# Kernel optimization log

Hardware: AMD Instinct MI355X
Metric: run time of the kernel (lower is better)

Reference implementation:

```python
import jax, jax.numpy as jnp
import numpy as np

HEADS = 4
DIM_HEAD = 32


def setup_inputs() -> dict:
    key = jax.random.key(0)
    k1, k2, k3 = jax.random.split(key, 3)
    b, c, d, h, w = 2, 64, 48, 48, 48
    hidden = HEADS * DIM_HEAD  # 128
    x = jax.random.normal(k1, (b, c, d, h, w), dtype=jnp.float32)
    # 1x1x1 convs are pointwise linear maps over channels
    w_qkv = jax.random.normal(k2, (hidden * 3, c), dtype=jnp.float32) * (1.0 / np.sqrt(c))
    w_out = jax.random.normal(k3, (c, hidden), dtype=jnp.float32) * (1.0 / np.sqrt(hidden))
    b_out = jnp.zeros((c,), dtype=jnp.float32)
    return {"x": x, "w_qkv": w_qkv, "w_out": w_out, "b_out": b_out}


def reference(x, w_qkv, w_out, b_out):
    b, c, d, h, w = x.shape
    n = d * h * w
    xf = x.reshape(b, c, n)                                # [b,c,n]
    qkv = jnp.einsum('oc,bcn->bon', w_qkv, xf)             # [b,3*heads*dh,n]
    qkv = qkv.reshape(b, 3, HEADS, DIM_HEAD, n)            # split order: qkv, heads, c
    q, k, v = qkv[:, 0], qkv[:, 1], qkv[:, 2]              # each [b,heads,dh,n]
    k = jax.nn.softmax(k, axis=-1)
    context = jnp.einsum('bhdn,bhen->bhde', k, v)          # [b,heads,dh,dh]
    out = jnp.einsum('bhde,bhdn->bhen', context, q)        # [b,heads,dh,n]
    out = out.reshape(b, HEADS * DIM_HEAD, n)
    out = jnp.einsum('co,bon->bcn', w_out, out) + b_out[None, :, None]
    return out.reshape(b, c, d, h, w)
```

## Files before the change

kernel.cpp:

```cpp
#include <hip/hip_runtime.h>
#include <stdint.h>


using f32x4 = __attribute__((ext_vector_type(4))) float;
using s16x8 = __attribute__((ext_vector_type(8))) short;

#define NSP 110592
#define NSHADOW 16
#define MFMA(a, b, c) __builtin_amdgcn_mfma_f32_16x16x32_bf16((a), (b), (c), 0, 0, 0)

static __device__ __forceinline__ unsigned short f2bf(float f) {
    return (unsigned short)((__float_as_uint(f) + 0x8000u) >> 16);
}

__global__ __launch_bounds__(256, 4) void k1z(
    const float* __restrict__ x, const float* __restrict__ wqkv,
    float* __restrict__ Sdst, float* __restrict__ Zdst, int mode)
{
    __shared__ unsigned short XT[64][68];
    __shared__ unsigned short EKV[4][2][32][40];
    const int tid = threadIdx.x;
    const int wv = tid >> 6;
    const int l = tid & 63;
    const int l15 = l & 15, l4 = l >> 4;
    const int blk = blockIdx.x;
    const int b = blk / 576;
    const int tbase = (blk % 576) * 6;
    const int h = wv;

    s16x8 afr[2][2][2];
    for (int kv = 0; kv < 2; ++kv)
        for (int mt = 0; mt < 2; ++mt)
            for (int s = 0; s < 2; ++s) {
                int row = 128 + kv * 128 + h * 32 + mt * 16 + l15;
                const float* wp = wqkv + row * 64 + s * 32 + l4 * 8;
                s16x8 a;
#pragma unroll
                for (int j = 0; j < 8; ++j) a[j] = (short)f2bf(wp[j]);
                afr[kv][mt][s] = a;
            }

    f32x4 sacc[2][2] = {};
    float zrow[8] = {};

    unsigned short (*EK)[40] = EKV[wv][0];
    unsigned short (*EV)[40] = EKV[wv][1];
    const float* xb = x + (size_t)b * 64 * NSP;

    const int c0 = tid >> 3;
    const int ng0 = (tid & 7) ^ (c0 & 7);
    const int c1 = (tid + 256) >> 3;
    const int ng1 = ((tid + 256) & 7) ^ (c1 & 7);

    float4 g0, g1;
    {
        const int n0 = tbase * 32;
        g0 = *(const float4*)(xb + (size_t)c0 * NSP + n0 + 4 * ng0);
        g1 = *(const float4*)(xb + (size_t)c1 * NSP + n0 + 4 * ng1);
    }

    for (int it = 0; it < 6; ++it) {
        if (it > 0) __syncthreads();
        {
            ushort4 u0, u1;
            u0.x = f2bf(g0.x); u0.y = f2bf(g0.y); u0.z = f2bf(g0.z); u0.w = f2bf(g0.w);
            u1.x = f2bf(g1.x); u1.y = f2bf(g1.y); u1.z = f2bf(g1.z); u1.w = f2bf(g1.w);
            *(ushort4*)&XT[c0][4 * ng0] = u0;
            *(ushort4*)&XT[c1][4 * ng1] = u1;
        }
        if (it < 5) {
            const int n0 = (tbase + it + 1) * 32;
            g0 = *(const float4*)(xb + (size_t)c0 * NSP + n0 + 4 * ng0);
            g1 = *(const float4*)(xb + (size_t)c1 * NSP + n0 + 4 * ng1);
        }
        __syncthreads();

        f32x4 ck[2][2] = {}, cv[2][2] = {};
#pragma unroll
        for (int s = 0; s < 2; ++s)
#pragma unroll
            for (int nt = 0; nt < 2; ++nt) {
                s16x8 bfr;
#pragma unroll
                for (int j = 0; j < 8; ++j)
                    bfr[j] = (short)XT[s * 32 + l4 * 8 + j][nt * 16 + l15];
#pragma unroll
                for (int mt = 0; mt < 2; ++mt) {
                    ck[mt][nt] = MFMA(afr[0][mt][s], bfr, ck[mt][nt]);
                    cv[mt][nt] = MFMA(afr[1][mt][s], bfr, cv[mt][nt]);
                }
            }
#pragma unroll
        for (int mt = 0; mt < 2; ++mt)
#pragma unroll
            for (int nt = 0; nt < 2; ++nt) {
                int col = nt * 16 + l15;
#pragma unroll
                for (int r = 0; r < 4; ++r) {
                    int row = mt * 16 + l4 * 4 + r;
                    float ek = __expf(ck[mt][nt][r]);
                    zrow[mt * 4 + r] += ek;
                    EK[row][col] = f2bf(ek);
                    EV[row][col] = f2bf(cv[mt][nt][r]);
                }
            }
#pragma unroll
        for (int td = 0; td < 2; ++td) {
            s16x8 a2 = *(const s16x8*)&EK[td * 16 + l15][l4 * 8];
#pragma unroll
            for (int te = 0; te < 2; ++te) {
                s16x8 b2 = *(const s16x8*)&EV[te * 16 + l15][l4 * 8];
                sacc[td][te] = MFMA(a2, b2, sacc[td][te]);
            }
        }
    }

#pragma unroll
    for (int i = 0; i < 8; ++i) {
        float z = zrow[i];
        z += __shfl_xor(z, 1);
        z += __shfl_xor(z, 2);
        z += __shfl_xor(z, 4);
        z += __shfl_xor(z, 8);
        zrow[i] = z;
    }

    if (mode == 0) {
        float* Zb = Zdst + (size_t)blk * 128;
        if (l15 == 0)
#pragma unroll
            for (int mt = 0; mt < 2; ++mt)
#pragma unroll
                for (int r = 0; r < 4; ++r)
                    Zb[h * 32 + mt * 16 + l4 * 4 + r] = zrow[mt * 4 + r];
        float* Sb = Sdst + (size_t)blk * 4096 + h * 1024;
#pragma unroll
        for (int td = 0; td < 2; ++td)
#pragma unroll
            for (int te = 0; te < 2; ++te)
#pragma unroll
                for (int r = 0; r < 4; ++r)
                    Sb[(td * 16 + l4 * 4 + r) * 32 + te * 16 + l15] =
                        sacc[td][te][r];
    } else {
        const int shadow = blk & (NSHADOW - 1);
        float* Zb = Zdst + (size_t)(shadow * 2 + b) * 128;
        if (l15 == 0)
#pragma unroll
            for (int mt = 0; mt < 2; ++mt)
#pragma unroll
                for (int r = 0; r < 4; ++r)
                    atomicAdd(&Zb[h * 32 + mt * 16 + l4 * 4 + r], zrow[mt * 4 + r]);
        float* Sb = Sdst + (size_t)(shadow * 2 + b) * 4096 + h * 1024;
#pragma unroll
        for (int td = 0; td < 2; ++td)
#pragma unroll
            for (int te = 0; te < 2; ++te)
#pragma unroll
                for (int r = 0; r < 4; ++r)
                    atomicAdd(&Sb[(td * 16 + l4 * 4 + r) * 32 + te * 16 + l15],
                              sacc[td][te][r]);
    }
}

__global__ __launch_bounds__(256) void k2pre(
    const float* __restrict__ Sp, const float* __restrict__ Zp,
    float* __restrict__ Ssh, float* __restrict__ Zsh)
{
    const int q = blockIdx.x & 3;
    const int b = (blockIdx.x >> 2) & 1;
    const int s = blockIdx.x >> 3;
    const int t = threadIdx.x;
    const int i = q * 1024 + t * 4;
    float4 acc = {0.f, 0.f, 0.f, 0.f};
#pragma unroll 6
    for (int j = 0; j < 36; ++j) {
        const float4 v =
            *(const float4*)&Sp[(size_t)(b * 576 + s + 16 * j) * 4096 + i];
        acc.x += v.x; acc.y += v.y; acc.z += v.z; acc.w += v.w;
    }
    *(float4*)&Ssh[(size_t)(s * 2 + b) * 4096 + i] = acc;
    if (q == 0 && t < 128) {
        float z = 0.f;
#pragma unroll 6
        for (int j = 0; j < 36; ++j)
            z += Zp[(size_t)(b * 576 + s + 16 * j) * 128 + t];
        Zsh[(size_t)(s * 2 + b) * 128 + t] = z;
    }
}

__global__ __launch_bounds__(1024) void k2s(
    const float* __restrict__ Ssh, const float* __restrict__ Zsh,
    const float* __restrict__ wout, const float* __restrict__ wqkv,
    unsigned short* __restrict__ WE)
{
    __shared__ float ctx[4][32][32];
    __shared__ float P[64][128];
    __shared__ float Zl[128];
    const int b = blockIdx.x;
    const int t = threadIdx.x;
    if (t < 128) {
        float z = 0.f;
#pragma unroll
        for (int s = 0; s < NSHADOW; ++s) z += Zsh[(size_t)(s * 2 + b) * 128 + t];
        Zl[t] = z;
    }
    __syncthreads();
    for (int i = t; i < 4096; i += 1024) {
        float sv = 0.f;
#pragma unroll
        for (int s = 0; s < NSHADOW; ++s) sv += Ssh[(size_t)(s * 2 + b) * 4096 + i];
        int h = i >> 10, d = (i >> 5) & 31;
        ctx[h][d][i & 31] = sv / Zl[h * 32 + d];
    }
    __syncthreads();
    for (int i = t; i < 8192; i += 1024) {
        int c = i >> 7, hd = i & 127, h = hd >> 5, d = hd & 31;
        const float* wo = wout + c * 128 + h * 32;
        float acc = 0.f;
#pragma unroll 8
        for (int e = 0; e < 32; ++e) acc += wo[e] * ctx[h][d][e];
        P[c][hd] = acc;
    }
    __syncthreads();
    for (int i = t; i < 4096; i += 1024) {
        int c = i >> 6, c2 = i & 63;
        float acc = 0.f;
#pragma unroll 8
        for (int hd = 0; hd < 128; ++hd) acc += P[c][hd] * wqkv[hd * 64 + c2];
        WE[b * 4096 + c * 64 + c2] = f2bf(acc);
    }
}

__global__ __launch_bounds__(256) void k3e(
    const float* __restrict__ x, const unsigned short* __restrict__ WE,
    const float* __restrict__ bout, float* __restrict__ out)
{
    const int tid = threadIdx.x;
    const int wv = tid >> 6;
    const int l = tid & 63;
    const int l15 = l & 15, l4 = l >> 4;
    const int b = blockIdx.x / 864;
    const int n0 = (blockIdx.x % 864) * 128;

    s16x8 afr[4][2];
#pragma unroll
    for (int mt = 0; mt < 4; ++mt)
#pragma unroll
        for (int s = 0; s < 2; ++s)
            afr[mt][s] = *(const s16x8*)(WE + b * 4096 + (mt * 16 + l15) * 64 + s * 32 + l4 * 8);

    float bias[4][4];
#pragma unroll
    for (int mt = 0; mt < 4; ++mt)
#pragma unroll
        for (int r = 0; r < 4; ++r) bias[mt][r] = bout[mt * 16 + l4 * 4 + r];

    const float* xb = x + (size_t)b * 64 * NSP;
    float* ob = out + (size_t)b * 64 * NSP;

    const int nq = wv * 32;
    const float* xq = xb + (size_t)(l4 * 8) * NSP + n0 + nq + l15;

    f32x4 acc[4][2] = {};
#pragma unroll
    for (int s = 0; s < 2; ++s) {
        float t0[8], t1[8];
#pragma unroll
        for (int j = 0; j < 8; ++j) {
            const float* p = xq + (size_t)(s * 32 + j) * NSP;
            t0[j] = p[0];
            t1[j] = p[16];
        }
        s16x8 b0, b1;
#pragma unroll
        for (int j = 0; j < 8; ++j) {
            b0[j] = (short)f2bf(t0[j]);
            b1[j] = (short)f2bf(t1[j]);
        }
#pragma unroll
        for (int mt = 0; mt < 4; ++mt) {
            acc[mt][0] = MFMA(afr[mt][s], b0, acc[mt][0]);
            acc[mt][1] = MFMA(afr[mt][s], b1, acc[mt][1]);
        }
    }

#pragma unroll
    for (int mt = 0; mt < 4; ++mt)
#pragma unroll
        for (int nt = 0; nt < 2; ++nt)
#pragma unroll
            for (int r = 0; r < 4; ++r)
                ob[(size_t)(mt * 16 + l4 * 4 + r) * NSP + n0 + nq + nt * 16 + l15] =
                    acc[mt][nt][r] + bias[mt][r];
}

extern "C" void kernel_launch(void* const* d_in, const int* in_sizes, int n_in,
                              void* d_out, int out_size, void* d_ws, size_t ws_size,
                              hipStream_t stream) {
    const float *x = nullptr, *wqkv = nullptr, *wout = nullptr, *bout = nullptr;
    for (int i = 0; i < n_in; ++i) {
        if (in_sizes[i] == 2 * 64 * NSP) x = (const float*)d_in[i];
        else if (in_sizes[i] == 384 * 64) wqkv = (const float*)d_in[i];
        else if (in_sizes[i] == 64 * 128) wout = (const float*)d_in[i];
        else if (in_sizes[i] == 64) bout = (const float*)d_in[i];
    }
    if (!x) x = (const float*)d_in[0];
    if (!wqkv) wqkv = (const float*)d_in[1];
    if (!wout) wout = (const float*)d_in[2];
    if (!bout) bout = (const float*)d_in[3];
    float* out = (float*)d_out;

    const size_t NEED_BIG = 20021248;
    if (ws_size >= NEED_BIG) {
        float* Sp = (float*)d_ws;
        float* Zp = (float*)((char*)d_ws + 18874368);
        float* Ssh = (float*)((char*)d_ws + 19464192);
        float* Zsh = (float*)((char*)d_ws + 19988480);
        unsigned short* WE = (unsigned short*)((char*)d_ws + 20004864);
        hipLaunchKernelGGL(k1z, dim3(1152), dim3(256), 0, stream, x, wqkv, Sp, Zp, 0);
        hipLaunchKernelGGL(k2pre, dim3(128), dim3(256), 0, stream, Sp, Zp, Ssh, Zsh);
        hipLaunchKernelGGL(k2s, dim3(2), dim3(1024), 0, stream, Ssh, Zsh, wout, wqkv, WE);
        hipLaunchKernelGGL(k3e, dim3(1728), dim3(256), 0, stream, x, WE, bout, out);
    } else {
        float* Ssh = (float*)d_ws;
        float* Zsh = (float*)((char*)d_ws + 524288);
        unsigned short* WE = (unsigned short*)((char*)d_ws + 540672);
        hipMemsetAsync(d_ws, 0, 540672, stream);
        hipLaunchKernelGGL(k1z, dim3(1152), dim3(256), 0, stream, x, wqkv, Ssh, Zsh, 1);
        hipLaunchKernelGGL(k2s, dim3(2), dim3(1024), 0, stream, Ssh, Zsh, wout, wqkv, WE);
        hipLaunchKernelGGL(k3e, dim3(1728), dim3(256), 0, stream, x, WE, bout, out);
    }
}
```

Before: 176.8 us.

## Split serial two-block context kernel into parallel context and weight-fold kernels

Replaces the two-block k2s kernel, which reduces shadow partial sums and folds the context through w_out and w_qkv on only two CUs, with two kernels. k2a uses 8 blocks to reduce the shadow partials into a normalized context, and k2b uses 128 blocks to compute the fused bf16 weight matrix one output channel at a time. This spreads a latency-bound serial stage across many CUs, at the cost of an extra launch and a small global round-trip for the context.

```diff
diff --git a/kernel.cpp b/kernel.cpp
--- a/kernel.cpp
+++ b/kernel.cpp
@@ -189,6 +189,61 @@
     }
 }
 
+__global__ __launch_bounds__(256) void k2a(
+    const float* __restrict__ Ssh, const float* __restrict__ Zsh,
+    float* __restrict__ ctxg)
+{
+    __shared__ float Zl[32];
+    const int b = blockIdx.x & 1;
+    const int h = blockIdx.x >> 1;
+    const int t = threadIdx.x;
+    if (t < 32) {
+        float z = 0.f;
+#pragma unroll
+        for (int s = 0; s < NSHADOW; ++s)
+            z += Zsh[(size_t)(s * 2 + b) * 128 + h * 32 + t];
+        Zl[t] = z;
+    }
+    __syncthreads();
+    const int li = t * 4;
+    const int d = li >> 5;
+    float4 sv = {0.f, 0.f, 0.f, 0.f};
+#pragma unroll
+    for (int s = 0; s < NSHADOW; ++s) {
+        const float4 v = *(const float4*)&Ssh[(size_t)(s * 2 + b) * 4096 + h * 1024 + li];
+        sv.x += v.x; sv.y += v.y; sv.z += v.z; sv.w += v.w;
+    }
+    const float zi = Zl[d];
+    sv.x /= zi; sv.y /= zi; sv.z /= zi; sv.w /= zi;
+    *(float4*)&ctxg[(size_t)(b * 4 + h) * 1024 + li] = sv;
+}
+
+__global__ __launch_bounds__(128) void k2b(
+    const float* __restrict__ ctxg, const float* __restrict__ wout,
+    const float* __restrict__ wqkv, unsigned short* __restrict__ WE)
+{
+    __shared__ float P[128];
+    const int b = blockIdx.x >> 6;
+    const int c = blockIdx.x & 63;
+    const int t = threadIdx.x;
+    {
+        const int h = t >> 5, d = t & 31;
+        const float* wo = wout + c * 128 + h * 32;
+        const float* cx = ctxg + (size_t)(b * 4 + h) * 1024 + d * 32;
+        float acc = 0.f;
+#pragma unroll 8
+        for (int e = 0; e < 32; ++e) acc += wo[e] * cx[e];
+        P[t] = acc;
+    }
+    __syncthreads();
+    if (t < 64) {
+        float acc = 0.f;
+#pragma unroll 8
+        for (int hd = 0; hd < 128; ++hd) acc += P[hd] * wqkv[hd * 64 + t];
+        WE[b * 4096 + c * 64 + t] = f2bf(acc);
+    }
+}
+
 __global__ __launch_bounds__(1024) void k2s(
     const float* __restrict__ Ssh, const float* __restrict__ Zsh,
     const float* __restrict__ wout, const float* __restrict__ wqkv,
@@ -311,16 +366,18 @@
     if (!bout) bout = (const float*)d_in[3];
     float* out = (float*)d_out;
 
-    const size_t NEED_BIG = 20021248;
+    const size_t NEED_BIG = 20054016;
     if (ws_size >= NEED_BIG) {
         float* Sp = (float*)d_ws;
         float* Zp = (float*)((char*)d_ws + 18874368);
         float* Ssh = (float*)((char*)d_ws + 19464192);
         float* Zsh = (float*)((char*)d_ws + 19988480);
         unsigned short* WE = (unsigned short*)((char*)d_ws + 20004864);
+        float* ctxg = (float*)((char*)d_ws + 20021248);
         hipLaunchKernelGGL(k1z, dim3(1152), dim3(256), 0, stream, x, wqkv, Sp, Zp, 0);
         hipLaunchKernelGGL(k2pre, dim3(128), dim3(256), 0, stream, Sp, Zp, Ssh, Zsh);
-        hipLaunchKernelGGL(k2s, dim3(2), dim3(1024), 0, stream, Ssh, Zsh, wout, wqkv, WE);
+        hipLaunchKernelGGL(k2a, dim3(8), dim3(256), 0, stream, Ssh, Zsh, ctxg);
+        hipLaunchKernelGGL(k2b, dim3(128), dim3(128), 0, stream, ctxg, wout, wqkv, WE);
         hipLaunchKernelGGL(k3e, dim3(1728), dim3(256), 0, stream, x, WE, bout, out);
     } else {
         float* Ssh = (float*)d_ws;
```

After: 154.0 us. 1.15x faster.
